# Kernel optimization log

Measured on AMD Instinct MI355X. Metric: run time of the kernel, lower is better.

Reference implementation:

```python
import jax, jax.numpy as jnp
import numpy as np

B, N, C, H = 8, 1024, 768, 12
WBITS, ABITS, PGABITS = 8, 8, 4
TH = 0.99  # greater-than mask threshold on MSB softmax


def quant(x, bits):
    """Fixed-point quantize to `bits` bits, straight-through estimator."""
    step = 2.0 ** (1 - bits)
    q = jnp.round(x / step) * step
    return x + jax.lax.stop_gradient(q - x)


def setup_inputs() -> dict:
    key = jax.random.key(0)
    k1, k2, k3 = jax.random.split(key, 3)
    x = jax.random.normal(k1, (B, N, C), jnp.float32)
    # qkv: QLinear(dim, 3*dim, bias=False); proj: QLinear(dim, dim, bias=True)
    w_qkv = jax.random.normal(k2, (3 * C, C), jnp.float32) * (C ** -0.5)
    w_proj = jax.random.normal(k3, (C, C), jnp.float32) * (C ** -0.5)
    b_proj = jnp.zeros((C,), jnp.float32)
    return {"x": x, "w_qkv": w_qkv, "w_proj": w_proj, "b_proj": b_proj}


def reference(x, w_qkv, w_proj, b_proj):
    d = C // H
    scale = d ** -0.5
    # QLinear: quantize activations and weights, then matmul (no qkv bias)
    qkv = quant(x, ABITS) @ quant(w_qkv, WBITS).T            # [B,N,3C]
    qkv = qkv.reshape(B, N, 3, H, d).transpose(2, 0, 3, 1, 4)  # [3,B,H,N,d]
    qkv = quant(qkv, ABITS)
    q, k, v = qkv[0], qkv[1], qkv[2]
    # low-precision MSB pass
    q_msb = quant(q, PGABITS)
    k_msb = quant(k, PGABITS)
    attn_msb = jax.nn.softmax(
        jnp.einsum('bhqd,bhkd->bhqk', q_msb, k_msb) * scale, axis=-1)
    # GreaterThan with straight-through backward (identity grad)
    gt = (attn_msb > TH).astype(attn_msb.dtype)
    mask = attn_msb + jax.lax.stop_gradient(gt - attn_msb)
    # full-precision pass, masked pre-softmax
    attn = jnp.einsum('bhqd,bhkd->bhqk', q, k) * scale * mask
    attn = quant(jax.nn.softmax(attn, axis=-1), ABITS)
    out = jnp.einsum('bhqk,bhkd->bhqd', attn, v)             # [B,H,N,d]
    out = out.transpose(0, 2, 1, 3).reshape(B, N, C)
    return quant(out, ABITS) @ quant(w_proj, WBITS).T + b_proj
```

## Files before the change

kernel.cpp:

```cpp
#include <hip/hip_runtime.h>

#define NB 8
#define NSEQ 1024
#define NC 768
#define NH 12
#define ND 64
#define NM 8192

typedef _Float16 v8h __attribute__((ext_vector_type(8)));
typedef float v4f __attribute__((ext_vector_type(4)));

__device__ __forceinline__ float q8f(float x){ return rintf(x*128.f)*0.0078125f; }
__device__ __forceinline__ float q4f(float x){ return rintf(x*8.f)*0.125f; }

__device__ __forceinline__ int swz(int r, int g){ return (r<<6) + (((g ^ (r & 7)) & 7)<<3); }

__device__ __forceinline__ void async_cp16(const _Float16* g, _Float16* l) {
  __builtin_amdgcn_global_load_lds(
      (const __attribute__((address_space(1))) unsigned int*)g,
      (__attribute__((address_space(3))) unsigned int*)l, 16, 0, 0);
}

__global__ __launch_bounds__(256) void k_pre(const float* __restrict__ x,
                                             const float* __restrict__ wq,
                                             const float* __restrict__ bias,
                                             _Float16* __restrict__ xt,
                                             _Float16* __restrict__ wqt,
                                             float* __restrict__ out) {
  int b = blockIdx.x;
  if (b < 3648) {
    const float* src; _Float16* dst; int gid;
    if (b < 3072) { src = x;  dst = xt;  gid = b*256 + threadIdx.x; }
    else          { src = wq; dst = wqt; gid = (b-3072)*256 + threadIdx.x; }
    int tile = gid / 12288;
    int rem  = gid - tile*12288;
    int chunk = rem >> 10, idx = rem & 1023;
    int r = idx >> 3, g = idx & 7;
    const float* s = src + (size_t)(tile*128 + r)*768 + chunk*64 + g*8;
    float4 v0 = *(const float4*)s, v1 = *(const float4*)(s + 4);
    v8h o;
    o[0]=(_Float16)q8f(v0.x); o[1]=(_Float16)q8f(v0.y); o[2]=(_Float16)q8f(v0.z); o[3]=(_Float16)q8f(v0.w);
    o[4]=(_Float16)q8f(v1.x); o[5]=(_Float16)q8f(v1.y); o[6]=(_Float16)q8f(v1.z); o[7]=(_Float16)q8f(v1.w);
    *(v8h*)&dst[((size_t)tile*12 + chunk)*8192 + swz(r, g)] = o;
  } else {
    int gid = (b - 3648)*256 + threadIdx.x;
    int c4 = gid % 192;
    ((float4*)out)[gid] = ((const float4*)bias)[c4];
  }
}

__device__ __forceinline__ void mfma_tile(const _Float16* Ah, const _Float16* Bh,
                                          int WR0, int l15, int quad, v4f acc[2][8]) {
#pragma unroll
  for (int ks = 0; ks < 2; ks++) {
    v8h a0 = *(const v8h*)&Ah[swz(WR0 + l15,      ks*4 + quad)];
    v8h a1 = *(const v8h*)&Ah[swz(WR0 + 16 + l15, ks*4 + quad)];
#pragma unroll
    for (int nt = 0; nt < 8; nt++) {
      v8h b = *(const v8h*)&Bh[swz(nt*16 + l15, ks*4 + quad)];
      acc[0][nt] = __builtin_amdgcn_mfma_f32_16x16x32_f16(a0, b, acc[0][nt], 0, 0, 0);
      acc[1][nt] = __builtin_amdgcn_mfma_f32_16x16x32_f16(a1, b, acc[1][nt], 0, 0, 0);
    }
  }
}

__global__ __launch_bounds__(256) void k_qk(const _Float16* __restrict__ xt,
                                            const _Float16* __restrict__ wqt,
                                            _Float16* __restrict__ Qm,
                                            _Float16* __restrict__ KmT) {
  __shared__ _Float16 S[16384];
  const int tid  = threadIdx.x;
  const int lane = tid & 63;
  const int quad = lane >> 4;
  const int l15  = lane & 15;
  const int wid  = tid >> 6;
  const int WR0  = wid * 32;
  const int m0 = blockIdx.x * 128, n0 = blockIdx.y * 128;
  const _Float16* Asrc = xt  + (size_t)blockIdx.x * 12 * 8192;
  const _Float16* Bsrc = wqt + (size_t)blockIdx.y * 12 * 8192;

  auto stage = [&](int kc) {
    const _Float16* a = Asrc + kc*8192;
    const _Float16* bsc = Bsrc + kc*8192;
#pragma unroll
    for (int s = 0; s < 8; s++) {
      int seg = wid*8 + s;
      const _Float16* g = (seg < 16 ? a + seg*512 : bsc + (seg-16)*512) + lane*8;
      async_cp16(g, &S[seg*512]);
    }
  };

  v4f acc[2][8] = {};
#pragma unroll 1
  for (int kc = 0; kc < 12; kc++) {
    stage(kc);
    __syncthreads();
    mfma_tile(&S[0], &S[8192], WR0, l15, quad, acc);
    __syncthreads();
  }

  const int which = (n0 >= 768);
  int c0 = n0 - which*768;
  _Float16* P = S;
#pragma unroll
  for (int half = 0; half < 2; half++) {
    if ((wid >> 1) == half) {
      int rl0 = (wid & 1)*32;
#pragma unroll
      for (int mt = 0; mt < 2; mt++)
#pragma unroll
        for (int nt = 0; nt < 8; nt++)
#pragma unroll
          for (int rr = 0; rr < 4; rr++) {
            float v = q8f(acc[mt][nt][rr]);
            float qm = (which == 0) ? q4f(v) * 0.125f : q4f(v);
            P[(rl0 + mt*16 + quad*4 + rr)*132 + nt*16 + l15] = (_Float16)qm;
          }
    }
    __syncthreads();
#pragma unroll
    for (int t = 0; t < 4; t++) {
      int idx = tid + t*256;
      int r = idx >> 4, cg = idx & 15;
      int m = m0 + half*64 + r;
      v8h val = *(const v8h*)&P[r*132 + cg*8];
      if (which == 0) {
        *(v8h*)&Qm[(size_t)m*768 + c0 + cg*8] = val;
      } else {
        int col = c0 + cg*8;
        int bI = m >> 10, n = m & 1023;
        int h = col >> 6, g = (col >> 3) & 7;
        size_t dst = ((size_t)(bI*NH + h)*16 + (n >> 6))*4096 + swz(n & 63, g);
        *(v8h*)&KmT[dst] = val;
      }
    }
    __syncthreads();
  }
}

__global__ __launch_bounds__(256) void k_attn(const _Float16* __restrict__ QmG,
                                              const _Float16* __restrict__ KmT,
                                              const float* __restrict__ x,
                                              const float* __restrict__ wqkv,
                                              const float* __restrict__ wproj,
                                              float* __restrict__ out) {
  __shared__ _Float16 S2[2][8192];
  __shared__ float rowm[128];
  __shared__ int   cand[128];
  __shared__ int   hrowA[128];
  __shared__ int   hcolA[128];
  __shared__ float qf[64], kf[64], vf[64];
  __shared__ float od[64];
  __shared__ float pps;
  __shared__ int   cnt, hcnt;

  const int tid  = threadIdx.x;
  const int lane = tid & 63;
  const int quad = lane >> 4;
  const int l15  = lane & 15;
  const int wid  = tid >> 6;
  const int R0   = wid * 16;
  const int bh = blockIdx.y;
  const int q0 = blockIdx.x * 128;
  const int bb = bh / NH, hb = bh % NH;
  const size_t mrow = (size_t)bb * NSEQ;
  const int hoff = hb * 64;
  const _Float16* KmB = KmT + (size_t)bh * 16 * 4096;

  if (tid == 0) { cnt = 0; hcnt = 0; }

  auto stageK2 = [&](int kp, int bi) {
#pragma unroll
    for (int s = 0; s < 4; s++) {
      int seg = wid*4 + s;
      async_cp16(KmB + kp*8192 + seg*512 + lane*8, &S2[bi][seg*512]);
    }
  };

  v8h aM[2][2];
#pragma unroll
  for (int b2 = 0; b2 < 2; b2++)
#pragma unroll
    for (int ks = 0; ks < 2; ks++)
      aM[b2][ks] = *(const v8h*)&QmG[(mrow + q0 + b2*64 + R0 + l15)*768 + hoff + ks*32 + quad*8];

  float lm[2][4], lm2[2][4];
#pragma unroll
  for (int b2 = 0; b2 < 2; b2++)
#pragma unroll
    for (int r = 0; r < 4; r++) { lm[b2][r] = -1e30f; lm2[b2][r] = -1e30f; }

  stageK2(0, 0);
#pragma unroll 1
  for (int kp = 0; kp < 8; kp++) {
    __syncthreads();
    if (kp + 1 < 8) stageK2(kp + 1, (kp + 1) & 1);
#pragma unroll
    for (int half = 0; half < 2; half++) {
      const _Float16* Kms = &S2[kp & 1][half*4096];
      v4f a0[4] = {}, a1[4] = {};
#pragma unroll
      for (int nt = 0; nt < 4; nt++)
#pragma unroll
        for (int ks = 0; ks < 2; ks++) {
          v8h b = *(const v8h*)&Kms[swz(l15 + 16*nt, ks*4 + quad)];
          a0[nt] = __builtin_amdgcn_mfma_f32_16x16x32_f16(aM[0][ks], b, a0[nt], 0, 0, 0);
          a1[nt] = __builtin_amdgcn_mfma_f32_16x16x32_f16(aM[1][ks], b, a1[nt], 0, 0, 0);
        }
#pragma unroll
      for (int r = 0; r < 4; r++) {
        float c0 = fmaxf(fmaxf(a0[0][r], a0[1][r]), fmaxf(a0[2][r], a0[3][r]));
        lm2[0][r] = fmaxf(lm2[0][r], fminf(lm[0][r], c0));
        lm[0][r]  = fmaxf(lm[0][r], c0);
        float c1 = fmaxf(fmaxf(a1[0][r], a1[1][r]), fmaxf(a1[2][r], a1[3][r]));
        lm2[1][r] = fmaxf(lm2[1][r], fminf(lm[1][r], c1));
        lm[1][r]  = fmaxf(lm[1][r], c1);
      }
    }
  }
#pragma unroll
  for (int b2 = 0; b2 < 2; b2++)
#pragma unroll
    for (int r = 0; r < 4; r++) {
      float m = lm[b2][r], m2 = lm2[b2][r];
#pragma unroll
      for (int o = 1; o < 16; o <<= 1) {
        float om  = __shfl_xor(m, o);
        float om2 = __shfl_xor(m2, o);
        m2 = fmaxf(fmaxf(m2, om2), fminf(m, om));
        m  = fmaxf(m, om);
      }
      if (l15 == 0 && (m - m2) > 4.5f) {
        int row = b2*64 + R0 + quad*4 + r;
        rowm[row] = m;
        int ix = atomicAdd(&cnt, 1);
        cand[ix] = row;
      }
    }
  __syncthreads();

  int nc = cnt;
  for (int ci = wid; ci < nc; ci += 4) {
    int row = cand[ci];
    float m = rowm[row];
    const _Float16* qrow = &QmG[(mrow + q0 + row)*768 + hoff];
    float l = 0.f, bmax = -1e30f;
    int bcol = 0;
    for (int t = 0; t < 16; t++) {
      float s = 0.f;
#pragma unroll
      for (int g = 0; g < 8; g++) {
        v8h qa = *(const v8h*)&qrow[g*8];
        v8h kb = *(const v8h*)&KmB[t*4096 + swz(lane, g)];
#pragma unroll
        for (int j = 0; j < 8; j++) s += (float)qa[j] * (float)kb[j];
      }
      l += expf(s - m);
      if (s > bmax) { bmax = s; bcol = t*64 + lane; }
    }
#pragma unroll
    for (int o = 1; o < 64; o <<= 1) {
      l += __shfl_xor(l, o);
      float ov = __shfl_xor(bmax, o);
      int   oc = __shfl_xor(bcol, o);
      if (ov > bmax || (ov == bmax && oc < bcol)) { bmax = ov; bcol = oc; }
    }
    if (lane == 0 && (1.0f / l) > 0.99f) {
      int ix = atomicAdd(&hcnt, 1);
      hrowA[ix] = row; hcolA[ix] = bcol;
    }
  }
  __syncthreads();

  int nh = hcnt;
  for (int hi = 0; hi < nh; hi++) {
    int row = hrowA[hi], cst = hcolA[hi];
    if (tid < 192) {
      int d = tid & 63, part = tid >> 6;
      int wrow = part*768 + hoff + d;
      int xrow = (part == 0) ? (int)(mrow + q0 + row) : (int)(mrow + cst);
      const float* xr = &x[(size_t)xrow*768];
      const float* wr = &wqkv[(size_t)wrow*768];
      float s = 0.f;
      for (int k = 0; k < 768; k++) s += q8f(xr[k]) * q8f(wr[k]);
      float v = q8f(s);
      if (part == 0) qf[d] = v; else if (part == 1) kf[d] = v; else vf[d] = v;
    }
    __syncthreads();
    if (tid == 0) {
      float s = 0.f;
      for (int d = 0; d < 64; d++) s += qf[d]*kf[d];
      float sf = s * 0.125f;
      float m2 = fmaxf(sf, 0.f);
      float l2 = expf(sf - m2) + 1023.f*expf(-m2);
      pps = rintf(expf(sf - m2)/l2*128.f)*0.0078125f;
    }
    __syncthreads();
    float p = pps;
    if (p != 0.f) {
      if (tid < 64) od[tid] = q8f(p * vf[tid]);
      __syncthreads();
      for (int c = tid; c < 768; c += 256) {
        const float* wr = &wproj[(size_t)c*768 + hoff];
        float s = 0.f;
        for (int d = 0; d < 64; d++) s += od[d] * q8f(wr[d]);
        atomicAdd(&out[(mrow + q0 + row)*768 + c], s);
      }
    }
    __syncthreads();
  }
}

extern "C" void kernel_launch(void* const* d_in, const int* in_sizes, int n_in,
                              void* d_out, int out_size, void* d_ws, size_t ws_size,
                              hipStream_t stream) {
  const float* x      = (const float*)d_in[0];
  const float* w_qkv  = (const float*)d_in[1];
  const float* w_proj = (const float*)d_in[2];
  const float* b_proj = (const float*)d_in[3];
  float* out = (float*)d_out;

  _Float16* p = (_Float16*)d_ws;
  _Float16* xt  = p;  p += (size_t)NM*768;
  _Float16* wqt = p;  p += (size_t)1536*768;
  _Float16* Qm  = p;  p += (size_t)NM*768;
  _Float16* KmT = p;  p += (size_t)NM*768;

  dim3 blk(256);
  k_pre <<<dim3(9792), blk, 0, stream>>>(x, w_qkv, b_proj, xt, wqt, out);
  k_qk  <<<dim3(64, 12), blk, 0, stream>>>(xt, wqt, Qm, KmT);
  k_attn<<<dim3( 8, 96), blk, 0, stream>>>(Qm, KmT, x, w_qkv, w_proj, out);
}
```

Baseline: 136.0 us.

## Fuse three kernels into one cooperative kernel with grid-wide syncs

Merges the preprocessing, QK projection GEMM and attention kernels into one cooperative launch of 768 blocks, separated by grid syncs, so the launch gaps between kernels go away. The preprocessing becomes a grid-stride loop and shared memory is reused across phases. If the cooperative launch fails, it falls back to three separate launches. The fused kernel is limited to the co-resident block count and pays for two grid barriers, and any imbalance in one phase now stalls the whole grid.

```diff
diff --git a/kernel.cpp b/kernel.cpp
--- a/kernel.cpp
+++ b/kernel.cpp
@@ -1,4 +1,7 @@
 #include <hip/hip_runtime.h>
+#include <hip/hip_cooperative_groups.h>
+
+namespace cg = cooperative_groups;
 
 #define NB 8
 #define NSEQ 1024
@@ -21,17 +24,28 @@
       (__attribute__((address_space(3))) unsigned int*)l, 16, 0, 0);
 }
 
-__global__ __launch_bounds__(256) void k_pre(const float* __restrict__ x,
-                                             const float* __restrict__ wq,
-                                             const float* __restrict__ bias,
-                                             _Float16* __restrict__ xt,
-                                             _Float16* __restrict__ wqt,
-                                             float* __restrict__ out) {
-  int b = blockIdx.x;
-  if (b < 3648) {
+struct AttnShared {
+  float rowm[128];
+  int   cand[128];
+  int   hrowA[128];
+  int   hcolA[128];
+  float qf[64], kf[64], vf[64], od[64];
+  float pps;
+  int   cnt, hcnt;
+};
+
+__device__ __forceinline__ void pre_body(int bid, int nb,
+                                         const float* __restrict__ x,
+                                         const float* __restrict__ wq,
+                                         const float* __restrict__ bias,
+                                         _Float16* __restrict__ xt,
+                                         _Float16* __restrict__ wqt,
+                                         float* __restrict__ out) {
+  const int step = nb*256;
+  for (int g0 = bid*256 + (int)threadIdx.x; g0 < 933888; g0 += step) {
     const float* src; _Float16* dst; int gid;
-    if (b < 3072) { src = x;  dst = xt;  gid = b*256 + threadIdx.x; }
-    else          { src = wq; dst = wqt; gid = (b-3072)*256 + threadIdx.x; }
+    if (g0 < 786432) { src = x;  dst = xt;  gid = g0; }
+    else             { src = wq; dst = wqt; gid = g0 - 786432; }
     int tile = gid / 12288;
     int rem  = gid - tile*12288;
     int chunk = rem >> 10, idx = rem & 1023;
@@ -42,11 +56,11 @@
     o[0]=(_Float16)q8f(v0.x); o[1]=(_Float16)q8f(v0.y); o[2]=(_Float16)q8f(v0.z); o[3]=(_Float16)q8f(v0.w);
     o[4]=(_Float16)q8f(v1.x); o[5]=(_Float16)q8f(v1.y); o[6]=(_Float16)q8f(v1.z); o[7]=(_Float16)q8f(v1.w);
     *(v8h*)&dst[((size_t)tile*12 + chunk)*8192 + swz(r, g)] = o;
-  } else {
-    int gid = (b - 3648)*256 + threadIdx.x;
-    int c4 = gid % 192;
-    ((float4*)out)[gid] = ((const float4*)bias)[c4];
-  }
+  }
+  const float4* b4 = (const float4*)bias;
+  float4* o4 = (float4*)out;
+  for (int i = bid*256 + (int)threadIdx.x; i < 1572864; i += step)
+    o4[i] = b4[i % 192];
 }
 
 __device__ __forceinline__ void mfma_tile(const _Float16* Ah, const _Float16* Bh,
@@ -64,36 +78,35 @@
   }
 }
 
-__global__ __launch_bounds__(256) void k_qk(const _Float16* __restrict__ xt,
-                                            const _Float16* __restrict__ wqt,
-                                            _Float16* __restrict__ Qm,
-                                            _Float16* __restrict__ KmT) {
-  __shared__ _Float16 S[16384];
+__device__ __forceinline__ void qk_body(int mblk, int nblk,
+                                        const _Float16* __restrict__ xt,
+                                        const _Float16* __restrict__ wqt,
+                                        _Float16* __restrict__ Qm,
+                                        _Float16* __restrict__ KmT,
+                                        _Float16* S) {
   const int tid  = threadIdx.x;
   const int lane = tid & 63;
   const int quad = lane >> 4;
   const int l15  = lane & 15;
   const int wid  = tid >> 6;
   const int WR0  = wid * 32;
-  const int m0 = blockIdx.x * 128, n0 = blockIdx.y * 128;
-  const _Float16* Asrc = xt  + (size_t)blockIdx.x * 12 * 8192;
-  const _Float16* Bsrc = wqt + (size_t)blockIdx.y * 12 * 8192;
-
-  auto stage = [&](int kc) {
-    const _Float16* a = Asrc + kc*8192;
-    const _Float16* bsc = Bsrc + kc*8192;
-#pragma unroll
-    for (int s = 0; s < 8; s++) {
-      int seg = wid*8 + s;
-      const _Float16* g = (seg < 16 ? a + seg*512 : bsc + (seg-16)*512) + lane*8;
-      async_cp16(g, &S[seg*512]);
-    }
-  };
+  const int m0 = mblk * 128, n0 = nblk * 128;
+  const _Float16* Asrc = xt  + (size_t)mblk * 12 * 8192;
+  const _Float16* Bsrc = wqt + (size_t)nblk * 12 * 8192;
 
   v4f acc[2][8] = {};
 #pragma unroll 1
   for (int kc = 0; kc < 12; kc++) {
-    stage(kc);
+    {
+      const _Float16* a = Asrc + kc*8192;
+      const _Float16* bsc = Bsrc + kc*8192;
+#pragma unroll
+      for (int s = 0; s < 8; s++) {
+        int seg = wid*8 + s;
+        const _Float16* g = (seg < 16 ? a + seg*512 : bsc + (seg-16)*512) + lane*8;
+        async_cp16(g, &S[seg*512]);
+      }
+    }
     __syncthreads();
     mfma_tile(&S[0], &S[8192], WR0, l15, quad, acc);
     __syncthreads();
@@ -138,42 +151,33 @@
   }
 }
 
-__global__ __launch_bounds__(256) void k_attn(const _Float16* __restrict__ QmG,
-                                              const _Float16* __restrict__ KmT,
-                                              const float* __restrict__ x,
-                                              const float* __restrict__ wqkv,
-                                              const float* __restrict__ wproj,
-                                              float* __restrict__ out) {
-  __shared__ _Float16 S2[2][8192];
-  __shared__ float rowm[128];
-  __shared__ int   cand[128];
-  __shared__ int   hrowA[128];
-  __shared__ int   hcolA[128];
-  __shared__ float qf[64], kf[64], vf[64];
-  __shared__ float od[64];
-  __shared__ float pps;
-  __shared__ int   cnt, hcnt;
-
+__device__ __forceinline__ void attn_body(int qblk, int bh,
+                                          const _Float16* __restrict__ QmG,
+                                          const _Float16* __restrict__ KmT,
+                                          const float* __restrict__ x,
+                                          const float* __restrict__ wqkv,
+                                          const float* __restrict__ wproj,
+                                          float* __restrict__ out,
+                                          _Float16* S2, AttnShared* A) {
   const int tid  = threadIdx.x;
   const int lane = tid & 63;
   const int quad = lane >> 4;
   const int l15  = lane & 15;
   const int wid  = tid >> 6;
   const int R0   = wid * 16;
-  const int bh = blockIdx.y;
-  const int q0 = blockIdx.x * 128;
+  const int q0 = qblk * 128;
   const int bb = bh / NH, hb = bh % NH;
   const size_t mrow = (size_t)bb * NSEQ;
   const int hoff = hb * 64;
   const _Float16* KmB = KmT + (size_t)bh * 16 * 4096;
 
-  if (tid == 0) { cnt = 0; hcnt = 0; }
+  if (tid == 0) { A->cnt = 0; A->hcnt = 0; }
 
   auto stageK2 = [&](int kp, int bi) {
 #pragma unroll
     for (int s = 0; s < 4; s++) {
       int seg = wid*4 + s;
-      async_cp16(KmB + kp*8192 + seg*512 + lane*8, &S2[bi][seg*512]);
+      async_cp16(KmB + kp*8192 + seg*512 + lane*8, &S2[bi*8192 + seg*512]);
     }
   };
 
@@ -197,7 +201,7 @@
     if (kp + 1 < 8) stageK2(kp + 1, (kp + 1) & 1);
 #pragma unroll
     for (int half = 0; half < 2; half++) {
-      const _Float16* Kms = &S2[kp & 1][half*4096];
+      const _Float16* Kms = &S2[(kp & 1)*8192 + half*4096];
       v4f a0[4] = {}, a1[4] = {};
 #pragma unroll
       for (int nt = 0; nt < 4; nt++)
@@ -232,17 +236,17 @@
       }
       if (l15 == 0 && (m - m2) > 4.5f) {
         int row = b2*64 + R0 + quad*4 + r;
-        rowm[row] = m;
-        int ix = atomicAdd(&cnt, 1);
-        cand[ix] = row;
+        A->rowm[row] = m;
+        int ix = atomicAdd(&A->cnt, 1);
+        A->cand[ix] = row;
       }
     }
   __syncthreads();
 
-  int nc = cnt;
+  int nc = A->cnt;
   for (int ci = wid; ci < nc; ci += 4) {
-    int row = cand[ci];
-    float m = rowm[row];
+    int row = A->cand[ci];
+    float m = A->rowm[row];
     const _Float16* qrow = &QmG[(mrow + q0 + row)*768 + hoff];
     float l = 0.f, bmax = -1e30f;
     int bcol = 0;
@@ -266,15 +270,15 @@
       if (ov > bmax || (ov == bmax && oc < bcol)) { bmax = ov; bcol = oc; }
     }
     if (lane == 0 && (1.0f / l) > 0.99f) {
-      int ix = atomicAdd(&hcnt, 1);
-      hrowA[ix] = row; hcolA[ix] = bcol;
+      int ix = atomicAdd(&A->hcnt, 1);
+      A->hrowA[ix] = row; A->hcolA[ix] = bcol;
     }
   }
   __syncthreads();
 
-  int nh = hcnt;
+  int nh = A->hcnt;
   for (int hi = 0; hi < nh; hi++) {
-    int row = hrowA[hi], cst = hcolA[hi];
+    int row = A->hrowA[hi], cst = A->hcolA[hi];
     if (tid < 192) {
       int d = tid & 63, part = tid >> 6;
       int wrow = part*768 + hoff + d;
@@ -284,31 +288,81 @@
       float s = 0.f;
       for (int k = 0; k < 768; k++) s += q8f(xr[k]) * q8f(wr[k]);
       float v = q8f(s);
-      if (part == 0) qf[d] = v; else if (part == 1) kf[d] = v; else vf[d] = v;
+      if (part == 0) A->qf[d] = v; else if (part == 1) A->kf[d] = v; else A->vf[d] = v;
     }
     __syncthreads();
     if (tid == 0) {
       float s = 0.f;
-      for (int d = 0; d < 64; d++) s += qf[d]*kf[d];
+      for (int d = 0; d < 64; d++) s += A->qf[d]*A->kf[d];
       float sf = s * 0.125f;
       float m2 = fmaxf(sf, 0.f);
       float l2 = expf(sf - m2) + 1023.f*expf(-m2);
-      pps = rintf(expf(sf - m2)/l2*128.f)*0.0078125f;
-    }
-    __syncthreads();
-    float p = pps;
+      A->pps = rintf(expf(sf - m2)/l2*128.f)*0.0078125f;
+    }
+    __syncthreads();
+    float p = A->pps;
     if (p != 0.f) {
-      if (tid < 64) od[tid] = q8f(p * vf[tid]);
+      if (tid < 64) A->od[tid] = q8f(p * A->vf[tid]);
       __syncthreads();
       for (int c = tid; c < 768; c += 256) {
         const float* wr = &wproj[(size_t)c*768 + hoff];
         float s = 0.f;
-        for (int d = 0; d < 64; d++) s += od[d] * q8f(wr[d]);
+        for (int d = 0; d < 64; d++) s += A->od[d] * q8f(wr[d]);
         atomicAdd(&out[(mrow + q0 + row)*768 + c], s);
       }
     }
     __syncthreads();
   }
+}
+
+__global__ __launch_bounds__(256, 3) void k_fused(const float* __restrict__ x,
+                                                  const float* __restrict__ wqkv,
+                                                  const float* __restrict__ wproj,
+                                                  const float* __restrict__ bias,
+                                                  float* __restrict__ out,
+                                                  _Float16* __restrict__ xt,
+                                                  _Float16* __restrict__ wqt,
+                                                  _Float16* __restrict__ Qm,
+                                                  _Float16* __restrict__ KmT) {
+  __shared__ __align__(16) _Float16 S[16384];
+  __shared__ AttnShared A;
+  const int bid = blockIdx.x;
+
+  pre_body(bid, 768, x, wqkv, bias, xt, wqt, out);
+  __threadfence();
+  cg::this_grid().sync();
+  qk_body(bid % 64, bid / 64, xt, wqt, Qm, KmT, S);
+  __threadfence();
+  cg::this_grid().sync();
+  attn_body(bid % 8, bid / 8, Qm, KmT, x, wqkv, wproj, out, S, &A);
+}
+
+__global__ __launch_bounds__(256) void k_pre(const float* __restrict__ x,
+                                             const float* __restrict__ wq,
+                                             const float* __restrict__ bias,
+                                             _Float16* __restrict__ xt,
+                                             _Float16* __restrict__ wqt,
+                                             float* __restrict__ out) {
+  pre_body(blockIdx.x, gridDim.x, x, wq, bias, xt, wqt, out);
+}
+
+__global__ __launch_bounds__(256) void k_qk(const _Float16* __restrict__ xt,
+                                            const _Float16* __restrict__ wqt,
+                                            _Float16* __restrict__ Qm,
+                                            _Float16* __restrict__ KmT) {
+  __shared__ __align__(16) _Float16 S[16384];
+  qk_body(blockIdx.x, blockIdx.y, xt, wqt, Qm, KmT, S);
+}
+
+__global__ __launch_bounds__(256) void k_attn(const _Float16* __restrict__ QmG,
+                                              const _Float16* __restrict__ KmT,
+                                              const float* __restrict__ x,
+                                              const float* __restrict__ wqkv,
+                                              const float* __restrict__ wproj,
+                                              float* __restrict__ out) {
+  __shared__ __align__(16) _Float16 S[16384];
+  __shared__ AttnShared A;
+  attn_body(blockIdx.x, blockIdx.y, QmG, KmT, x, wqkv, wproj, out, S, &A);
 }
 
 extern "C" void kernel_launch(void* const* d_in, const int* in_sizes, int n_in,
@@ -326,8 +380,15 @@
   _Float16* Qm  = p;  p += (size_t)NM*768;
   _Float16* KmT = p;  p += (size_t)NM*768;
 
-  dim3 blk(256);
-  k_pre <<<dim3(9792), blk, 0, stream>>>(x, w_qkv, b_proj, xt, wqt, out);
-  k_qk  <<<dim3(64, 12), blk, 0, stream>>>(xt, wqt, Qm, KmT);
-  k_attn<<<dim3( 8, 96), blk, 0, stream>>>(Qm, KmT, x, w_qkv, w_proj, out);
-}
+  void* kargs[] = {(void*)&x, (void*)&w_qkv, (void*)&w_proj, (void*)&b_proj,
+                   (void*)&out, (void*)&xt, (void*)&wqt, (void*)&Qm, (void*)&KmT};
+  hipError_t e = hipLaunchCooperativeKernel((const void*)k_fused, dim3(768),
+                                            dim3(256), kargs, 0, stream);
+  if (e != hipSuccess) {
+    (void)hipGetLastError();
+    dim3 blk(256);
+    k_pre <<<dim3(768),    blk, 0, stream>>>(x, w_qkv, b_proj, xt, wqt, out);
+    k_qk  <<<dim3(64, 12), blk, 0, stream>>>(xt, wqt, Qm, KmT);
+    k_attn<<<dim3( 8, 96), blk, 0, stream>>>(Qm, KmT, x, w_qkv, w_proj, out);
+  }
+}
```

Measured after the change: 430.5 us. 216% more time.
